# Performance work log

Hardware: AMD Instinct MI355X
Metric: run time of the kernel (lower is better)

Reference implementation:

```python
import jax, jax.numpy as jnp
import numpy as np
from math import log

X_SIZE, Y_SIZE, W_SIZE = 512, 512, 256
SIGMA = 2.0
TIME_CONST = 1000.0 / log(SIGMA)  # default time_constant = 1000/log(sigma)


def setup_inputs() -> dict:
    key = jax.random.key(0)
    k1, k2 = jax.random.split(key)
    x = jax.random.normal(k1, (W_SIZE,), dtype=jnp.float32)
    W = jax.random.normal(k2, (X_SIZE, Y_SIZE, W_SIZE), dtype=jnp.float32)
    return {"x": x, "W": W, "time_step": 100}


def reference(x, W, time_step):
    # per-cell L2 distance: (X_SIZE, Y_SIZE)
    d = jnp.linalg.norm(x - W, ord=2, axis=-1)
    flat = jnp.argmin(d)
    wx, wy = jnp.unravel_index(flat, (X_SIZE, Y_SIZE))
    # torch.meshgrid default 'ij' indexing
    GX, GY = jnp.meshgrid(
        jnp.arange(X_SIZE, dtype=jnp.float32),
        jnp.arange(Y_SIZE, dtype=jnp.float32),
        indexing="ij",
    )
    decay = SIGMA * jnp.exp(-jnp.float32(time_step) / TIME_CONST)
    denom = 2.0 * decay * decay
    # Faithful to torch: GX.T[wx, wy] == wy and GY.T[wx, wy] == wx
    distx = (GX - wy.astype(jnp.float32)) ** 2
    disty = (GY - wx.astype(jnp.float32)) ** 2
    h = (jnp.exp(-distx / denom) * jnp.exp(-disty / denom)).T
    return h, (wx, wy)
```

## Files before the change

### kernel.cpp

```cpp
#include <hip/hip_runtime.h>
#include <math.h>

#define XS 512
#define YS 512
#define WDIM 256
#define NCELLS (XS * YS)
#define K1_BLOCKS 2048
#define K1_THREADS 256

typedef float vfloat4 __attribute__((ext_vector_type(4)));

__global__ __launch_bounds__(K1_THREADS) void som_dist_kernel(
    const float* __restrict__ x,
    const float* __restrict__ W,
    unsigned long long* __restrict__ ws) {
  const int lane = threadIdx.x & 63;
  const int waveInBlock = threadIdx.x >> 6;
  const int gw = blockIdx.x * (K1_THREADS / 64) + waveInBlock;

  const vfloat4 xv = ((const vfloat4*)x)[lane];

  float bestD = 3.4e38f;
  int bestI = 0;

  const int base = gw * 32;
#pragma unroll 8
  for (int c = 0; c < 32; ++c) {
    const int cell = base + c;
    const vfloat4* p = (const vfloat4*)(W + (size_t)cell * WDIM) + lane;
    const vfloat4 wv = __builtin_nontemporal_load(p);
    const float dx = xv.x - wv.x;
    const float dy = xv.y - wv.y;
    const float dz = xv.z - wv.z;
    const float dw = xv.w - wv.w;
    float s = dx * dx + dy * dy + dz * dz + dw * dw;
#pragma unroll
    for (int off = 32; off > 0; off >>= 1) s += __shfl_xor(s, off, 64);
    if (s < bestD) { bestD = s; bestI = cell; }
  }

  const unsigned long long packed =
      ((unsigned long long)__float_as_uint(bestD) << 32) | (unsigned int)bestI;

  __shared__ unsigned long long sbest[K1_THREADS / 64];
  if (lane == 0) sbest[waveInBlock] = packed;
  __syncthreads();
  if (threadIdx.x == 0) {
    unsigned long long m = sbest[0];
#pragma unroll
    for (int i = 1; i < K1_THREADS / 64; ++i) {
      const unsigned long long v = sbest[i];
      m = (v < m) ? v : m;
    }
    atomicMin(ws, m);
  }
}

__global__ __launch_bounds__(256) void som_h_kernel(
    const unsigned long long* __restrict__ ws,
    const int* __restrict__ time_step,
    float* __restrict__ out) {
  const int t = threadIdx.x;
  const unsigned long long packed = *ws;
  const int flat = (int)(packed & 0xFFFFFFFFULL);
  const int wx = flat >> 9;
  const int wy = flat & (YS - 1);

  const float ts = (float)(*time_step);
  const float TIME_CONST = 1442.6950408889634f;
  const float decay = 2.0f * expf(-ts / TIME_CONST);
  const float denom = 2.0f * decay * decay;
  const float inv = -1.0f / denom;

  const int e = blockIdx.x * 1024 + t * 4;
  const int i = e >> 9;
  const int j0 = e & (YS - 1);
  const float di = (float)(i - wx);
  const float di2 = di * di;

  const float d0 = (float)(j0 + 0 - wy);
  const float d1 = (float)(j0 + 1 - wy);
  const float d2 = (float)(j0 + 2 - wy);
  const float d3 = (float)(j0 + 3 - wy);
  vfloat4 r;
  r.x = expf((di2 + d0 * d0) * inv);
  r.y = expf((di2 + d1 * d1) * inv);
  r.z = expf((di2 + d2 * d2) * inv);
  r.w = expf((di2 + d3 * d3) * inv);
  ((vfloat4*)out)[e >> 2] = r;

  if (blockIdx.x == 0 && t == 0) {
    out[NCELLS] = (float)wx;
    out[NCELLS + 1] = (float)wy;
  }
}

extern "C" void kernel_launch(void* const* d_in, const int* in_sizes, int n_in,
                              void* d_out, int out_size, void* d_ws, size_t ws_size,
                              hipStream_t stream) {
  const float* x = (const float*)d_in[0];
  const float* W = (const float*)d_in[1];
  const int* ts = (const int*)d_in[2];
  float* out = (float*)d_out;
  unsigned long long* ws = (unsigned long long*)d_ws;

  (void)hipMemsetAsync(ws, 0xFF, 8, stream);
  som_dist_kernel<<<K1_BLOCKS, K1_THREADS, 0, stream>>>(x, W, ws);
  som_h_kernel<<<NCELLS / 1024, 256, 0, stream>>>(ws, ts, out);
}
```

Before: 347.8 us.

## Double-buffer W loads, transpose-reduce 8 cells per wave, spread atomics across slots

The distance kernel now prefetches the next batch of 8 rows into registers while computing the current batch, so more loads are in flight per wave. It replaces eight separate 6-step butterfly reductions with a transpose-style reduction that sums 8 cells together, which cuts the number of shuffles. The final atomicMin is spread over 32 padded slots to reduce contention on one address, and the second kernel combines the slots with a wave shuffle. In exchange it uses more registers and adds a wider memset and a slot reduction in every block of the second kernel.

```diff
diff --git a/kernel.cpp b/kernel.cpp
--- a/kernel.cpp
+++ b/kernel.cpp
@@ -7,6 +7,8 @@
 #define NCELLS (XS * YS)
 #define K1_BLOCKS 2048
 #define K1_THREADS 256
+#define NSLOTS 32
+#define SLOT_STRIDE 16
 
 typedef float vfloat4 __attribute__((ext_vector_type(4)));
 
@@ -24,23 +26,84 @@
   int bestI = 0;
 
   const int base = gw * 32;
-#pragma unroll 8
-  for (int c = 0; c < 32; ++c) {
-    const int cell = base + c;
-    const vfloat4* p = (const vfloat4*)(W + (size_t)cell * WDIM) + lane;
-    const vfloat4 wv = __builtin_nontemporal_load(p);
-    const float dx = xv.x - wv.x;
-    const float dy = xv.y - wv.y;
-    const float dz = xv.z - wv.z;
-    const float dw = xv.w - wv.w;
-    float s = dx * dx + dy * dy + dz * dz + dw * dw;
+  const int r7 = lane & 7;
+
+  const bool b0 = (lane & 1) != 0;
+  const bool b1 = (lane & 2) != 0;
+  const bool b2 = (lane & 4) != 0;
+
+  vfloat4 buf[2][8];
+
+  {
+    const vfloat4* p0 = (const vfloat4*)(W + (size_t)base * WDIM) + lane;
 #pragma unroll
-    for (int off = 32; off > 0; off >>= 1) s += __shfl_xor(s, off, 64);
-    if (s < bestD) { bestD = s; bestI = cell; }
+    for (int r = 0; r < 8; ++r)
+      buf[0][r] = __builtin_nontemporal_load(p0 + r * (WDIM / 4));
   }
 
-  const unsigned long long packed =
+#pragma unroll
+  for (int b = 0; b < 4; ++b) {
+    if (b < 3) {
+      const vfloat4* pn =
+          (const vfloat4*)(W + (size_t)(base + (b + 1) * 8) * WDIM) + lane;
+#pragma unroll
+      for (int r = 0; r < 8; ++r)
+        buf[(b + 1) & 1][r] = __builtin_nontemporal_load(pn + r * (WDIM / 4));
+    }
+
+    const int cb = base + b * 8;
+    float s[8];
+#pragma unroll
+    for (int r = 0; r < 8; ++r) {
+      const vfloat4 wv = buf[b & 1][r];
+      const float dx = xv.x - wv.x;
+      const float dy = xv.y - wv.y;
+      const float dz = xv.z - wv.z;
+      const float dw = xv.w - wv.w;
+      s[r] = dx * dx + dy * dy + dz * dz + dw * dw;
+    }
+
+    float t0, t1, t2, t3;
+    {
+      float k, sd;
+      k = b0 ? s[1] : s[0]; sd = b0 ? s[0] : s[1];
+      t0 = k + __shfl_xor(sd, 1, 64);
+      k = b0 ? s[3] : s[2]; sd = b0 ? s[2] : s[3];
+      t1 = k + __shfl_xor(sd, 1, 64);
+      k = b0 ? s[5] : s[4]; sd = b0 ? s[4] : s[5];
+      t2 = k + __shfl_xor(sd, 1, 64);
+      k = b0 ? s[7] : s[6]; sd = b0 ? s[6] : s[7];
+      t3 = k + __shfl_xor(sd, 1, 64);
+    }
+    float u0, u1;
+    {
+      float k, sd;
+      k = b1 ? t1 : t0; sd = b1 ? t0 : t1;
+      u0 = k + __shfl_xor(sd, 2, 64);
+      k = b1 ? t3 : t2; sd = b1 ? t2 : t3;
+      u1 = k + __shfl_xor(sd, 2, 64);
+    }
+    float v;
+    {
+      const float k = b2 ? u1 : u0;
+      const float sd = b2 ? u0 : u1;
+      v = k + __shfl_xor(sd, 4, 64);
+    }
+    v += __shfl_xor(v, 8, 64);
+    v += __shfl_xor(v, 16, 64);
+    v += __shfl_xor(v, 32, 64);
+
+    if (v < bestD) { bestD = v; bestI = cb + r7; }
+  }
+
+  unsigned long long packed =
       ((unsigned long long)__float_as_uint(bestD) << 32) | (unsigned int)bestI;
+
+#pragma unroll
+  for (int off = 32; off > 0; off >>= 1) {
+    const unsigned long long o = __shfl_xor(packed, off, 64);
+    packed = (o < packed) ? o : packed;
+  }
 
   __shared__ unsigned long long sbest[K1_THREADS / 64];
   if (lane == 0) sbest[waveInBlock] = packed;
@@ -49,10 +112,10 @@
     unsigned long long m = sbest[0];
 #pragma unroll
     for (int i = 1; i < K1_THREADS / 64; ++i) {
-      const unsigned long long v = sbest[i];
-      m = (v < m) ? v : m;
+      const unsigned long long v2 = sbest[i];
+      m = (v2 < m) ? v2 : m;
     }
-    atomicMin(ws, m);
+    atomicMin(ws + (blockIdx.x & (NSLOTS - 1)) * SLOT_STRIDE, m);
   }
 }
 
@@ -61,8 +124,16 @@
     const int* __restrict__ time_step,
     float* __restrict__ out) {
   const int t = threadIdx.x;
-  const unsigned long long packed = *ws;
-  const int flat = (int)(packed & 0xFFFFFFFFULL);
+  const int lane = t & 63;
+
+  unsigned long long v = ws[(lane & (NSLOTS - 1)) * SLOT_STRIDE];
+#pragma unroll
+  for (int off = 1; off < 32; off <<= 1) {
+    const unsigned long long o = __shfl_xor(v, off, 64);
+    v = (o < v) ? o : v;
+  }
+
+  const int flat = (int)(v & 0xFFFFFFFFULL);
   const int wx = flat >> 9;
   const int wy = flat & (YS - 1);
 
@@ -104,7 +175,7 @@
   float* out = (float*)d_out;
   unsigned long long* ws = (unsigned long long*)d_ws;
 
-  (void)hipMemsetAsync(ws, 0xFF, 8, stream);
+  (void)hipMemsetAsync(ws, 0xFF, NSLOTS * SLOT_STRIDE * 8, stream);
   som_dist_kernel<<<K1_BLOCKS, K1_THREADS, 0, stream>>>(x, W, ws);
   som_h_kernel<<<NCELLS / 1024, 256, 0, stream>>>(ws, ts, out);
 }
```

Result: faster. 339.8 us, median of 2 (-2.3%).
